# Optimization experiments

Hardware: AMD Instinct MI355X
Metric: run time of the kernel (lower is better)

The kernel has to match this reference:

```python
import jax, jax.numpy as jnp
import numpy as np

B, N, F = 256, 64, 64
S = 2 * N + 2  # seq_len = N*2 + 2 = 130
EPS = 1e-6
SCALE = float(np.sqrt(S))


def _norm(x, alpha, beta):
    # custom Norm: mean/std over last axis, affine params shaped (F, S)
    m = jnp.mean(x, axis=-1, keepdims=True)
    s = jnp.std(x, axis=-1, keepdims=True)
    return alpha * (x - m) / (s + EPS) + beta


def setup_inputs() -> dict:
    key = jax.random.key(0)
    ks = jax.random.split(key, 12)
    d = {
        "sp": jax.random.normal(ks[0], (B, F), jnp.float32),
        "h1": jax.random.normal(ks[1], (B, N, F), jnp.float32),
        "h2": jax.random.normal(ks[2], (B, N, F), jnp.float32),
        # Dense(seq_len) kernels act on last axis of length S
        "Wq": jax.random.normal(ks[3], (S, S), jnp.float32) * 0.05,
        "bq": jnp.zeros((S,), jnp.float32),
        "Wk": jax.random.normal(ks[4], (S, S), jnp.float32) * 0.05,
        "bk": jnp.zeros((S,), jnp.float32),
        "Wv": jax.random.normal(ks[5], (S, S), jnp.float32) * 0.05,
        "bv": jnp.zeros((S,), jnp.float32),
        "alpha1": jnp.ones((F, S), jnp.float32),
        "beta1": jnp.zeros((F, S), jnp.float32),
        "alpha2": jnp.ones((F, S), jnp.float32),
        "beta2": jnp.zeros((F, S), jnp.float32),
        "Wlin": jax.random.normal(ks[6], (F * S, 1), jnp.float32) * 0.02,
        "blin": jnp.zeros((1,), jnp.float32),
    }
    return d


def reference(sp, h1, h2, Wq, bq, Wk, bk, Wv, bv,
              alpha1, beta1, alpha2, beta2, Wlin, blin):
    # obs: (B, 2N+1, F) -> transpose -> (B, F, 2N+1)
    obs = jnp.concatenate((h1, h2, sp[:, None, :]), axis=1).transpose(0, 2, 1)
    h2t = h2.transpose(0, 2, 1)  # (B, F, N): each action is a (B, F) column

    def fwd_action(action):  # action: (B, F)
        x = jnp.concatenate((obs, action[:, :, None]), axis=-1)  # (B, F, S)
        xn = _norm(x, alpha1, beta1)
        q = xn @ Wq + bq  # (B, F, S)
        k = xn @ Wk + bk
        v = xn @ Wv + bv
        # attention over the FEATURE axis: scores (B, F, F)
        sim = jnp.einsum('bis,bjs->bij', q, k) / SCALE
        p = jax.nn.softmax(sim, axis=-1)
        ao = jnp.einsum('bij,bjs->bis', p, v)  # (B, F, S)
        # deterministic dropout => residual is ao + ao
        y = _norm(ao + ao, alpha2, beta2)
        return y.reshape(B, -1) @ Wlin + blin  # (B, 1)

    q_values = jax.vmap(fwd_action, in_axes=-1, out_axes=1)(h2t)  # (B, N, 1)
    return q_values.reshape(B, N)
```

## Files before the change

kernel.cpp:

```cpp
#include <hip/hip_runtime.h>
#include <math.h>


typedef __attribute__((ext_vector_type(4))) float f32x4;
typedef __attribute__((ext_vector_type(8))) _Float16 h8;

#define EPSF 1e-6f
#define INVS 0.0877058019307029f

__device__ __forceinline__ unsigned short f2h(float f) {
  _Float16 h = (_Float16)f;
  return __builtin_bit_cast(unsigned short, h);
}
__device__ __forceinline__ float h2f(unsigned short s) {
  return (float)__builtin_bit_cast(_Float16, s);
}
__device__ __forceinline__ unsigned int pkh(float a, float b) {
  unsigned int r;
  asm("v_cvt_pkrtz_f16_f32 %0, %1, %2" : "=v"(r) : "v"(a), "v"(b));
  return r;
}

__global__ __launch_bounds__(256) void k0(
    const float* __restrict__ alpha1, const float* __restrict__ beta1,
    const float* __restrict__ alpha2, const float* __restrict__ beta2,
    const float* __restrict__ Wq, const float* __restrict__ bq,
    const float* __restrict__ Wk, const float* __restrict__ bk,
    const float* __restrict__ Wv, const float* __restrict__ bv,
    const float* __restrict__ Wlin, const float* __restrict__ blin,
    unsigned short* __restrict__ ABqk, unsigned short* __restrict__ ABv,
    unsigned short* __restrict__ AWt, float* __restrict__ Paw, float* __restrict__ Ccw)
{
  __shared__ float sbuf[64 * 132];
  __shared__ float Wbuf[130 * 144];
  int blk = blockIdx.x, tid = threadIdx.x;
  if (blk < 6) {
    int m = blk >> 1, isB = blk & 1;
    const float* src  = isB ? beta1 : alpha1;
    const float* W    = (m == 0) ? Wq : (m == 1) ? Wk : Wv;
    const float* bias = (m == 0) ? bq : (m == 1) ? bk : bv;
    for (int e = tid; e < 8320; e += 256) { int f = e / 130, s = e - f * 130; sbuf[f * 132 + s] = src[e]; }
    for (int e = tid; e < 16900; e += 256) { int s = e / 130, t = e - s * 130; Wbuf[s * 144 + t] = W[e]; }
    __syncthreads();
    int ty = tid >> 4, tx = tid & 15;
    float acc[4][9] = {};
    for (int s = 0; s < 130; ++s) {
      float g0 = sbuf[(ty * 4 + 0) * 132 + s];
      float g1 = sbuf[(ty * 4 + 1) * 132 + s];
      float g2 = sbuf[(ty * 4 + 2) * 132 + s];
      float g3 = sbuf[(ty * 4 + 3) * 132 + s];
#pragma unroll
      for (int c = 0; c < 9; ++c) {
        float wv = Wbuf[s * 144 + tx + 16 * c];
        acc[0][c] += g0 * wv; acc[1][c] += g1 * wv;
        acc[2][c] += g2 * wv; acc[3][c] += g3 * wv;
      }
    }
#pragma unroll
    for (int i = 0; i < 4; ++i)
      for (int c = 0; c < 9; ++c) {
        int t = tx + 16 * c;
        if (t < 136) {
          float val = (t < 130) ? (acc[i][c] + (isB ? bias[t] : 0.f)) : 0.f;
          unsigned short v16 = f2h(val);
          int f = ty * 4 + i;
          if (m == 2) ABv[t * 128 + isB * 64 + f] = v16;
          else        ABqk[(m * 64 + f) * 272 + (t >> 3) * 16 + isB * 8 + (t & 7)] = v16;
        }
      }
  } else if (blk == 6) {
    if (tid < 64) {
      int f = tid;
      float pa = 0.f, cc = 0.f;
      for (int s = 0; s < 130; ++s) {
        float wl = Wlin[f * 130 + s];
        float aw = alpha2[f * 130 + s] * wl;
        AWt[s * 72 + f] = f2h(aw);
        pa += aw;
        cc += beta2[f * 130 + s] * wl;
      }
      for (int s = 130; s < 144; ++s) AWt[s * 72 + f] = 0;
      Paw[f] = pa;
#pragma unroll
      for (int msk = 1; msk <= 32; msk <<= 1) cc += __shfl_xor(cc, msk, 64);
      if (f == 0) Ccw[0] = cc + blin[0];
    }
  }
}

__global__ __launch_bounds__(256) void k1(
    const float* __restrict__ h1, const float* __restrict__ h2,
    const float* __restrict__ sp, const float* __restrict__ alpha1,
    const float* __restrict__ Wq, const float* __restrict__ Wk, const float* __restrict__ Wv,
    unsigned short* __restrict__ UqkB, unsigned short* __restrict__ UvB,
    float* __restrict__ S1g, float* __restrict__ S2g)
{
  __shared__ float gbuf[64 * 132];
  __shared__ float Wbuf[130 * 144];
  __shared__ float ps[2][256];
  int b = blockIdx.x, tid = threadIdx.x;
  float s1 = 0.f, s2 = 0.f;
  for (int idx = tid; idx < 8256; idx += 256) {
    int s = idx >> 6, f = idx & 63;
    float x = (s < 64)  ? h1[((size_t)(b * 64 + s)) * 64 + f]
            : (s < 128) ? h2[((size_t)(b * 64 + (s - 64))) * 64 + f]
                        : sp[b * 64 + f];
    gbuf[f * 132 + s] = alpha1[f * 130 + s] * x;
    s1 += x; s2 += x * x;
  }
  ps[0][tid] = s1; ps[1][tid] = s2;
  __syncthreads();
  if (tid < 64) {
    S1g[b * 64 + tid] = ps[0][tid] + ps[0][tid + 64] + ps[0][tid + 128] + ps[0][tid + 192];
    S2g[b * 64 + tid] = ps[1][tid] + ps[1][tid + 64] + ps[1][tid + 128] + ps[1][tid + 192];
  }
  int ty = tid >> 4, tx = tid & 15;
  for (int m = 0; m < 3; ++m) {
    const float* W = (m == 0) ? Wq : (m == 1) ? Wk : Wv;
    __syncthreads();
    for (int e = tid; e < 16900; e += 256) { int s = e / 130, t = e - s * 130; Wbuf[s * 144 + t] = W[e]; }
    __syncthreads();
    float acc[4][9] = {};
    for (int s = 0; s < 129; ++s) {
      float g0 = gbuf[(ty * 4 + 0) * 132 + s];
      float g1 = gbuf[(ty * 4 + 1) * 132 + s];
      float g2 = gbuf[(ty * 4 + 2) * 132 + s];
      float g3 = gbuf[(ty * 4 + 3) * 132 + s];
#pragma unroll
      for (int c = 0; c < 9; ++c) {
        float wv = Wbuf[s * 144 + tx + 16 * c];
        acc[0][c] += g0 * wv; acc[1][c] += g1 * wv;
        acc[2][c] += g2 * wv; acc[3][c] += g3 * wv;
      }
    }
#pragma unroll
    for (int i = 0; i < 4; ++i)
      for (int c = 0; c < 9; ++c) {
        int t = tx + 16 * c;
        if (t < 136) {
          unsigned short v16 = f2h((t < 130) ? acc[i][c] : 0.f);
          int f = ty * 4 + i;
          if (m == 2) UvB[((size_t)b * 136 + t) * 64 + f] = v16;
          else        UqkB[(((size_t)b * 2 + m) * 64 + f) * 136 + t] = v16;
        }
      }
  }
}

__global__ __launch_bounds__(512, 2) void k2(
    const float* __restrict__ h2, const float* __restrict__ alpha1,
    const unsigned short* __restrict__ UqkB, const unsigned short* __restrict__ UvB,
    const unsigned short* __restrict__ ABqk, const unsigned short* __restrict__ ABv,
    const unsigned short* __restrict__ AWt,
    const float* __restrict__ S1g, const float* __restrict__ S2g,
    const float* __restrict__ Paw, const float* __restrict__ Ccw,
    const float* __restrict__ Wq, const float* __restrict__ Wk, const float* __restrict__ Wv,
    float* __restrict__ out)
{
  __shared__ __align__(16) unsigned short qb[64 * 168];
  __shared__ __align__(16) unsigned short kb[64 * 168];
  __shared__ __align__(16) unsigned short vT[144 * 72];
  __shared__ __align__(16) unsigned short pb[64 * 72];
  __shared__ __align__(16) unsigned short uqk_l[2 * 64 * 136];
  __shared__ __align__(16) unsigned short uv_l[136 * 64];
  __shared__ __align__(16) unsigned short w129h[3][136];
  __shared__ float S1l[64], S2l[64], ael[64];
  __shared__ __align__(16) unsigned short mrow[64], irow[64], crow[64];
  __shared__ float redbuf[4];

  int b = blockIdx.x, tid = threadIdx.x;
  int w = tid >> 6, l = tid & 63, l15 = l & 15, l4 = l >> 4;

  if (tid < 136) {
    w129h[0][tid] = (tid < 130) ? f2h(Wq[129 * 130 + tid]) : (unsigned short)0;
    w129h[1][tid] = (tid < 130) ? f2h(Wk[129 * 130 + tid]) : (unsigned short)0;
    w129h[2][tid] = (tid < 130) ? f2h(Wv[129 * 130 + tid]) : (unsigned short)0;
  }
  if (tid >= 256 && tid < 320) {
    int ff = tid - 256;
    float s1v = S1g[b * 64 + ff];
    float s2v = S2g[b * 64 + ff];
    float aev = alpha1[ff * 130 + 129];
    S1l[ff] = s1v; S2l[ff] = s2v; ael[ff] = aev;
    float a  = h2[((size_t)(b * 64 + 0)) * 64 + ff];
    float m  = (s1v + a) * (1.f / 130.f);
    float e2 = (s2v + a * a) * (1.f / 130.f);
    float sd = sqrtf(fmaxf(e2 - m * m, 0.f));
    mrow[ff] = f2h(m);
    irow[ff] = f2h(1.f / (sd + EPSF));
    crow[ff] = f2h(aev * a);
  }
  {
    const uint4* src = (const uint4*)(UqkB + ((size_t)b * 2) * 64 * 136);
    uint4* dst = (uint4*)uqk_l;
    for (int i = tid; i < 2176; i += 512) dst[i] = src[i];
  }
  {
    const uint4* src = (const uint4*)(UvB + (size_t)b * 136 * 64);
    uint4* dst = (uint4*)uv_l;
    for (int i = tid; i < 1088; i += 512) dst[i] = src[i];
  }
  for (int i = tid; i < 64 * 24; i += 512) {
    int ff = i / 24, t = 136 + (i - ff * 24);
    qb[ff * 168 + t] = 0; kb[ff * 168 + t] = 0;
  }
  for (int i = tid; i < 14 * 72; i += 512) vT[130 * 72 + i] = 0;

  float awr[9][4], pawr[4];
  if (w < 4) {
#pragma unroll
    for (int sf = 0; sf < 9; ++sf)
#pragma unroll
      for (int rr = 0; rr < 4; ++rr)
        awr[sf][rr] = h2f(AWt[(sf * 16 + l15) * 72 + w * 16 + l4 * 4 + rr]);
#pragma unroll
    for (int rr = 0; rr < 4; ++rr) pawr[rr] = Paw[w * 16 + l4 * 4 + rr];
  }
  float ccv = Ccw[0];

  int isK = tid >> 8, t5 = tid & 255;
  const unsigned short* abg = ABqk + isK * 64 * 272;
  unsigned short* dstqk = isK ? kb : qb;

  __syncthreads();

  auto genqk = [&](int o) {
    int fo = o / 17, g = o - fo * 17;
    _Float16 m = __builtin_bit_cast(_Float16, mrow[fo]);
    _Float16 inv = __builtin_bit_cast(_Float16, irow[fo]);
    _Float16 c = __builtin_bit_cast(_Float16, crow[fo]);
    h8 uu = *(const h8*)(uqk_l + (isK * 64 + fo) * 136 + g * 8);
    h8 aa = *(const h8*)(abg + fo * 272 + g * 16);
    h8 bb = *(const h8*)(abg + fo * 272 + g * 16 + 8);
    h8 ww = *(const h8*)(&w129h[isK][g * 8]);
    h8 res = (uu + c * ww - m * aa) * inv + bb;
    *(h8*)(dstqk + fo * 168 + g * 8) = res;
  };
  auto genv = [&](int o) {
    int t = o >> 3, vf = o & 7;
    _Float16 wv = __builtin_bit_cast(_Float16, w129h[2][t]);
    h8 uu = *(const h8*)(uv_l + t * 64 + vf * 8);
    h8 aa = *(const h8*)(ABv + t * 128 + vf * 8);
    h8 bb = *(const h8*)(ABv + t * 128 + 64 + vf * 8);
    h8 mv = *(const h8*)(&mrow[vf * 8]);
    h8 iv = *(const h8*)(&irow[vf * 8]);
    h8 cv = *(const h8*)(&crow[vf * 8]);
    h8 res = (uu + cv * wv - mv * aa) * iv + bb;
    *(h8*)(&vT[t * 72 + vf * 8]) = res;
  };

  for (int n = 0; n < 64; ++n) {
    if (n > 0 && tid == 0)
      out[b * 64 + n - 1] = redbuf[0] + redbuf[1] + redbuf[2] + redbuf[3] + ccv;
#pragma unroll
    for (int kg = 0; kg < 4; ++kg) genqk(t5 + (kg << 8));
    if (t5 < 64) genqk(1024 + t5);
    genv(tid); genv(tid + 512);
    if (tid < 16) genv(1024 + tid);
    __syncthreads();

    if (w < 4) {
      f32x4 sacc[4] = {};
      {
        const unsigned short* qrow = &qb[(w * 16 + l15) * 168 + l4 * 8];
#pragma unroll
        for (int kk = 0; kk < 5; ++kk) {
          h8 avv = *(const h8*)&qrow[kk * 32];
#pragma unroll
          for (int cf = 0; cf < 4; ++cf) {
            h8 bvv = *(const h8*)&kb[(cf * 16 + l15) * 168 + l4 * 8 + kk * 32];
            sacc[cf] = __builtin_amdgcn_mfma_f32_16x16x32_f16(avv, bvv, sacc[cf], 0, 0, 0);
          }
        }
      }
      float prob[4][4];
#pragma unroll
      for (int rr = 0; rr < 4; ++rr) {
        float ssum = 0.f;
#pragma unroll
        for (int cf = 0; cf < 4; ++cf) {
          float e = __expf(sacc[cf][rr] * INVS);
          prob[cf][rr] = e;
          ssum += e;
        }
#pragma unroll
        for (int msk = 1; msk <= 8; msk <<= 1) ssum += __shfl_xor(ssum, msk, 64);
        float is = 1.f / ssum;
#pragma unroll
        for (int cf = 0; cf < 4; ++cf) prob[cf][rr] *= is;
      }
#pragma unroll
      for (int cf = 0; cf < 4; ++cf) {
        unsigned int p01 = pkh(prob[cf][0], prob[cf][1]);
        unsigned int p23 = pkh(prob[cf][2], prob[cf][3]);
        int base = (w * 16 + l4 * 4) * 72 + cf * 16 + l15;
        pb[base]       = (unsigned short)p01;
        pb[base + 72]  = (unsigned short)(p01 >> 16);
        pb[base + 144] = (unsigned short)p23;
        pb[base + 216] = (unsigned short)(p23 >> 16);
      }

      f32x4 ao[9] = {};
      {
        const unsigned short* prow = &pb[(w * 16 + l15) * 72 + l4 * 8];
#pragma unroll
        for (int kk = 0; kk < 2; ++kk) {
          h8 avv = *(const h8*)&prow[kk * 32];
#pragma unroll
          for (int sf = 0; sf < 9; ++sf) {
            h8 bvv = *(const h8*)&vT[(sf * 16 + l15) * 72 + l4 * 8 + kk * 32];
            ao[sf] = __builtin_amdgcn_mfma_f32_16x16x32_f16(avv, bvv, ao[sf], 0, 0, 0);
          }
        }
      }
      float csum = 0.f;
#pragma unroll
      for (int rr = 0; rr < 4; ++rr) {
        float s1 = 0.f, s2 = 0.f, sdt = 0.f;
#pragma unroll
        for (int sf = 0; sf < 9; ++sf) {
          float v = ao[sf][rr];
          s1 += v; s2 += v * v; sdt += v * awr[sf][rr];
        }
#pragma unroll
        for (int msk = 1; msk <= 8; msk <<= 1) {
          s1 += __shfl_xor(s1, msk, 64);
          s2 += __shfl_xor(s2, msk, 64);
          sdt += __shfl_xor(sdt, msk, 64);
        }
        float mz  = 2.f * s1 * (1.f / 130.f);
        float ez2 = 4.f * s2 * (1.f / 130.f);
        float sg  = sqrtf(fmaxf(ez2 - mz * mz, 0.f));
        float i2  = 1.f / (sg + EPSF);
        csum += (2.f * sdt - mz * pawr[rr]) * i2;
      }
      csum += __shfl_xor(csum, 16, 64);
      csum += __shfl_xor(csum, 32, 64);
      if (l == 0) redbuf[w] = csum;
    } else if (w == 4 && n < 63) {
      int ff = l;
      float a  = h2[((size_t)(b * 64 + n + 1)) * 64 + ff];
      float m  = (S1l[ff] + a) * (1.f / 130.f);
      float e2 = (S2l[ff] + a * a) * (1.f / 130.f);
      float sd = sqrtf(fmaxf(e2 - m * m, 0.f));
      mrow[ff] = f2h(m);
      irow[ff] = f2h(1.f / (sd + EPSF));
      crow[ff] = f2h(ael[ff] * a);
    }
    __syncthreads();
  }
  if (tid == 0)
    out[b * 64 + 63] = redbuf[0] + redbuf[1] + redbuf[2] + redbuf[3] + ccv;
}

extern "C" void kernel_launch(void* const* d_in, const int* in_sizes, int n_in,
                              void* d_out, int out_size, void* d_ws, size_t ws_size,
                              hipStream_t stream) {
  const float* sp     = (const float*)d_in[0];
  const float* h1     = (const float*)d_in[1];
  const float* h2     = (const float*)d_in[2];
  const float* Wq     = (const float*)d_in[3];
  const float* bq     = (const float*)d_in[4];
  const float* Wk     = (const float*)d_in[5];
  const float* bk     = (const float*)d_in[6];
  const float* Wv     = (const float*)d_in[7];
  const float* bv     = (const float*)d_in[8];
  const float* alpha1 = (const float*)d_in[9];
  const float* beta1  = (const float*)d_in[10];
  const float* alpha2 = (const float*)d_in[11];
  const float* beta2  = (const float*)d_in[12];
  const float* Wlin   = (const float*)d_in[13];
  const float* blin   = (const float*)d_in[14];
  float* out = (float*)d_out;

  unsigned short* UqkB = (unsigned short*)d_ws;
  unsigned short* UvB  = UqkB + 4456448;
  unsigned short* ABqk = UvB + 2228224;
  unsigned short* ABv  = ABqk + 34816;
  unsigned short* AWt  = ABv + 17408;
  float* S1g = (float*)(AWt + 10368);
  float* S2g = S1g + 16384;
  float* Paw = S2g + 16384;
  float* Ccw = Paw + 64;

  k0<<<dim3(7), dim3(256), 0, stream>>>(alpha1, beta1, alpha2, beta2,
                                        Wq, bq, Wk, bk, Wv, bv, Wlin, blin,
                                        ABqk, ABv, AWt, Paw, Ccw);
  k1<<<dim3(256), dim3(256), 0, stream>>>(h1, h2, sp, alpha1, Wq, Wk, Wv,
                                          UqkB, UvB, S1g, S2g);
  k2<<<dim3(256), dim3(512), 0, stream>>>(h2, alpha1, UqkB, UvB, ABqk, ABv, AWt,
                                          S1g, S2g, Paw, Ccw,
                                          Wq, Wk, Wv, out);
}
```

Baseline: 327.3 us.

## Split k2 action loop across two blocks per batch and keep U/AB operands in registers

The main kernel now launches two blocks per batch row, each handling 32 of the 64 actions, so 512 blocks instead of 256 fill the GPU's compute units better. The per-batch U and AB operands used to build q/k/v are loaded once into registers before the loop instead of being staged in shared memory and reread every iteration. This cuts LDS footprint and per-iteration LDS reads. The cost is duplicated setup loads per block and higher register pressure under the 512-thread, 2-blocks-per-CU launch bound, which could cause spills.

Measured after the change: 343.5 us. +5.0%, slower.

```diff
diff --git a/kernel.cpp b/kernel.cpp
--- a/kernel.cpp
+++ b/kernel.cpp
@@ -161,14 +161,14 @@
   __shared__ __align__(16) unsigned short kb[64 * 168];
   __shared__ __align__(16) unsigned short vT[144 * 72];
   __shared__ __align__(16) unsigned short pb[64 * 72];
-  __shared__ __align__(16) unsigned short uqk_l[2 * 64 * 136];
-  __shared__ __align__(16) unsigned short uv_l[136 * 64];
   __shared__ __align__(16) unsigned short w129h[3][136];
   __shared__ float S1l[64], S2l[64], ael[64];
   __shared__ __align__(16) unsigned short mrow[64], irow[64], crow[64];
   __shared__ float redbuf[4];
 
-  int b = blockIdx.x, tid = threadIdx.x;
+  int bh = blockIdx.x;
+  int b = bh >> 1, n0 = (bh & 1) << 5;
+  int tid = threadIdx.x;
   int w = tid >> 6, l = tid & 63, l15 = l & 15, l4 = l >> 4;
 
   if (tid < 136) {
@@ -182,23 +182,13 @@
     float s2v = S2g[b * 64 + ff];
     float aev = alpha1[ff * 130 + 129];
     S1l[ff] = s1v; S2l[ff] = s2v; ael[ff] = aev;
-    float a  = h2[((size_t)(b * 64 + 0)) * 64 + ff];
+    float a  = h2[((size_t)(b * 64 + n0)) * 64 + ff];
     float m  = (s1v + a) * (1.f / 130.f);
     float e2 = (s2v + a * a) * (1.f / 130.f);
     float sd = sqrtf(fmaxf(e2 - m * m, 0.f));
     mrow[ff] = f2h(m);
     irow[ff] = f2h(1.f / (sd + EPSF));
-    crow[ff] = f2h(aev * a);
-  }
-  {
-    const uint4* src = (const uint4*)(UqkB + ((size_t)b * 2) * 64 * 136);
-    uint4* dst = (uint4*)uqk_l;
-    for (int i = tid; i < 2176; i += 512) dst[i] = src[i];
-  }
-  {
-    const uint4* src = (const uint4*)(UvB + (size_t)b * 136 * 64);
-    uint4* dst = (uint4*)uv_l;
-    for (int i = tid; i < 1088; i += 512) dst[i] = src[i];
+    crow[ff] = f2h(ael[ff] * a);
   }
   for (int i = tid; i < 64 * 24; i += 512) {
     int ff = i / 24, t = 136 + (i - ff * 24);
@@ -219,29 +209,48 @@
   float ccv = Ccw[0];
 
   int isK = tid >> 8, t5 = tid & 255;
-  const unsigned short* abg = ABqk + isK * 64 * 272;
+  const unsigned short* uqkg = UqkB + ((size_t)b * 2 + isK) * 64 * 136;
+  const unsigned short* abg  = ABqk + isK * 64 * 272;
+  const unsigned short* uvg  = UvB + (size_t)b * 136 * 64;
   unsigned short* dstqk = isK ? kb : qb;
 
+  auto ldu = [&](int o) { int fo = o / 17, g = o - fo * 17;
+                          return *(const h8*)(uqkg + fo * 136 + g * 8); };
+  auto lda = [&](int o) { int fo = o / 17, g = o - fo * 17;
+                          return *(const h8*)(abg + fo * 272 + g * 16); };
+  auto ldb = [&](int o) { int fo = o / 17, g = o - fo * 17;
+                          return *(const h8*)(abg + fo * 272 + g * 16 + 8); };
+  h8 qU0 = ldu(t5),       qA0 = lda(t5),       qB0 = ldb(t5);
+  h8 qU1 = ldu(t5 + 256), qA1 = lda(t5 + 256), qB1 = ldb(t5 + 256);
+  h8 qU2 = ldu(t5 + 512), qA2 = lda(t5 + 512), qB2 = ldb(t5 + 512);
+  h8 qU3 = ldu(t5 + 768), qA3 = lda(t5 + 768), qB3 = ldb(t5 + 768);
+  h8 qUt = {}, qAt = {}, qBt = {};
+  if (t5 < 64) { qUt = ldu(1024 + t5); qAt = lda(1024 + t5); qBt = ldb(1024 + t5); }
+  auto ldvu = [&](int o) { int t = o >> 3, vf = o & 7;
+                           return *(const h8*)(uvg + t * 64 + vf * 8); };
+  auto ldva = [&](int o) { int t = o >> 3, vf = o & 7;
+                           return *(const h8*)(ABv + t * 128 + (o & 7) * 8); };
+  auto ldvb = [&](int o) { int t = o >> 3;
+                           return *(const h8*)(ABv + t * 128 + 64 + (o & 7) * 8); };
+  h8 vU0 = ldvu(tid),       vA0 = ldva(tid),       vB0 = ldvb(tid);
+  h8 vU1 = ldvu(tid + 512), vA1 = ldva(tid + 512), vB1 = ldvb(tid + 512);
+  h8 vUt = {}, vAt = {}, vBt = {};
+  if (tid < 16) { vUt = ldvu(1024 + tid); vAt = ldva(1024 + tid); vBt = ldvb(1024 + tid); }
+
   __syncthreads();
 
-  auto genqk = [&](int o) {
+  auto genqk = [&](int o, h8 uu, h8 aa, h8 bb) {
     int fo = o / 17, g = o - fo * 17;
-    _Float16 m = __builtin_bit_cast(_Float16, mrow[fo]);
+    _Float16 m   = __builtin_bit_cast(_Float16, mrow[fo]);
     _Float16 inv = __builtin_bit_cast(_Float16, irow[fo]);
-    _Float16 c = __builtin_bit_cast(_Float16, crow[fo]);
-    h8 uu = *(const h8*)(uqk_l + (isK * 64 + fo) * 136 + g * 8);
-    h8 aa = *(const h8*)(abg + fo * 272 + g * 16);
-    h8 bb = *(const h8*)(abg + fo * 272 + g * 16 + 8);
+    _Float16 c   = __builtin_bit_cast(_Float16, crow[fo]);
     h8 ww = *(const h8*)(&w129h[isK][g * 8]);
     h8 res = (uu + c * ww - m * aa) * inv + bb;
     *(h8*)(dstqk + fo * 168 + g * 8) = res;
   };
-  auto genv = [&](int o) {
+  auto genv = [&](int o, h8 uu, h8 aa, h8 bb) {
     int t = o >> 3, vf = o & 7;
     _Float16 wv = __builtin_bit_cast(_Float16, w129h[2][t]);
-    h8 uu = *(const h8*)(uv_l + t * 64 + vf * 8);
-    h8 aa = *(const h8*)(ABv + t * 128 + vf * 8);
-    h8 bb = *(const h8*)(ABv + t * 128 + 64 + vf * 8);
     h8 mv = *(const h8*)(&mrow[vf * 8]);
     h8 iv = *(const h8*)(&irow[vf * 8]);
     h8 cv = *(const h8*)(&crow[vf * 8]);
@@ -249,14 +258,17 @@
     *(h8*)(&vT[t * 72 + vf * 8]) = res;
   };
 
-  for (int n = 0; n < 64; ++n) {
-    if (n > 0 && tid == 0)
+  for (int n = n0; n < n0 + 32; ++n) {
+    if (n > n0 && tid == 0)
       out[b * 64 + n - 1] = redbuf[0] + redbuf[1] + redbuf[2] + redbuf[3] + ccv;
-#pragma unroll
-    for (int kg = 0; kg < 4; ++kg) genqk(t5 + (kg << 8));
-    if (t5 < 64) genqk(1024 + t5);
-    genv(tid); genv(tid + 512);
-    if (tid < 16) genv(1024 + tid);
+    genqk(t5,       qU0, qA0, qB0);
+    genqk(t5 + 256, qU1, qA1, qB1);
+    genqk(t5 + 512, qU2, qA2, qB2);
+    genqk(t5 + 768, qU3, qA3, qB3);
+    if (t5 < 64) genqk(1024 + t5, qUt, qAt, qBt);
+    genv(tid,       vU0, vA0, vB0);
+    genv(tid + 512, vU1, vA1, vB1);
+    if (tid < 16) genv(1024 + tid, vUt, vAt, vBt);
     __syncthreads();
 
     if (w < 4) {
@@ -337,7 +349,7 @@
       csum += __shfl_xor(csum, 16, 64);
       csum += __shfl_xor(csum, 32, 64);
       if (l == 0) redbuf[w] = csum;
-    } else if (w == 4 && n < 63) {
+    } else if (w == 4 && n < n0 + 31) {
       int ff = l;
       float a  = h2[((size_t)(b * 64 + n + 1)) * 64 + ff];
       float m  = (S1l[ff] + a) * (1.f / 130.f);
@@ -350,7 +362,7 @@
     __syncthreads();
   }
   if (tid == 0)
-    out[b * 64 + 63] = redbuf[0] + redbuf[1] + redbuf[2] + redbuf[3] + ccv;
+    out[b * 64 + n0 + 31] = redbuf[0] + redbuf[1] + redbuf[2] + redbuf[3] + ccv;
 }
 
 extern "C" void kernel_launch(void* const* d_in, const int* in_sizes, int n_in,
@@ -388,7 +400,7 @@
                                         ABqk, ABv, AWt, Paw, Ccw);
   k1<<<dim3(256), dim3(256), 0, stream>>>(h1, h2, sp, alpha1, Wq, Wk, Wv,
                                           UqkB, UvB, S1g, S2g);
-  k2<<<dim3(256), dim3(512), 0, stream>>>(h2, alpha1, UqkB, UvB, ABqk, ABv, AWt,
+  k2<<<dim3(512), dim3(512), 0, stream>>>(h2, alpha1, UqkB, UvB, ABqk, ABv, AWt,
                                           S1g, S2g, Paw, Ccw,
                                           Wq, Wk, Wv, out);
 }
```

## Split k2 across four blocks per batch and keep U operands in registers

Applied to the files above, without the earlier changes.

k2 now launches 1024 blocks of 256 threads, and each block handles 16 of the 64 actions for one batch element instead of all 64. The per-action norm statistics are computed up front for all 16 actions, which removes the dedicated warp that prepared the next action. The U slices for q, k and v are loaded straight from global memory into registers rather than staged in LDS, which cuts shared-memory use and allows more blocks per CU. In exchange each block reloads the U data and weights, so global traffic for them rises fourfold and register pressure grows.

New measurement: 383.6 us. +17.2%, slower.

```diff
diff --git a/kernel.cpp b/kernel.cpp
--- a/kernel.cpp
+++ b/kernel.cpp
@@ -147,7 +147,7 @@
   }
 }
 
-__global__ __launch_bounds__(512, 2) void k2(
+__global__ __launch_bounds__(256, 2) void k2(
     const float* __restrict__ h2, const float* __restrict__ alpha1,
     const unsigned short* __restrict__ UqkB, const unsigned short* __restrict__ UvB,
     const unsigned short* __restrict__ ABqk, const unsigned short* __restrict__ ABv,
@@ -161,14 +161,15 @@
   __shared__ __align__(16) unsigned short kb[64 * 168];
   __shared__ __align__(16) unsigned short vT[144 * 72];
   __shared__ __align__(16) unsigned short pb[64 * 72];
-  __shared__ __align__(16) unsigned short uqk_l[2 * 64 * 136];
-  __shared__ __align__(16) unsigned short uv_l[136 * 64];
   __shared__ __align__(16) unsigned short w129h[3][136];
-  __shared__ float S1l[64], S2l[64], ael[64];
-  __shared__ __align__(16) unsigned short mrow[64], irow[64], crow[64];
+  __shared__ __align__(16) unsigned short mrowA[16][64];
+  __shared__ __align__(16) unsigned short irowA[16][64];
+  __shared__ __align__(16) unsigned short crowA[16][64];
   __shared__ float redbuf[4];
 
-  int b = blockIdx.x, tid = threadIdx.x;
+  int bh = blockIdx.x;
+  int b = bh >> 2, n0 = (bh & 3) << 4;
+  int tid = threadIdx.x;
   int w = tid >> 6, l = tid & 63, l15 = l & 15, l4 = l >> 4;
 
   if (tid < 136) {
@@ -176,90 +177,112 @@
     w129h[1][tid] = (tid < 130) ? f2h(Wk[129 * 130 + tid]) : (unsigned short)0;
     w129h[2][tid] = (tid < 130) ? f2h(Wv[129 * 130 + tid]) : (unsigned short)0;
   }
-  if (tid >= 256 && tid < 320) {
-    int ff = tid - 256;
+  for (int idx = tid; idx < 16 * 64; idx += 256) {
+    int nn = idx >> 6, ff = idx & 63;
+    float a   = h2[((size_t)(b * 64 + n0 + nn)) * 64 + ff];
     float s1v = S1g[b * 64 + ff];
     float s2v = S2g[b * 64 + ff];
     float aev = alpha1[ff * 130 + 129];
-    S1l[ff] = s1v; S2l[ff] = s2v; ael[ff] = aev;
-    float a  = h2[((size_t)(b * 64 + 0)) * 64 + ff];
-    float m  = (s1v + a) * (1.f / 130.f);
-    float e2 = (s2v + a * a) * (1.f / 130.f);
-    float sd = sqrtf(fmaxf(e2 - m * m, 0.f));
-    mrow[ff] = f2h(m);
-    irow[ff] = f2h(1.f / (sd + EPSF));
-    crow[ff] = f2h(aev * a);
-  }
-  {
-    const uint4* src = (const uint4*)(UqkB + ((size_t)b * 2) * 64 * 136);
-    uint4* dst = (uint4*)uqk_l;
-    for (int i = tid; i < 2176; i += 512) dst[i] = src[i];
-  }
-  {
-    const uint4* src = (const uint4*)(UvB + (size_t)b * 136 * 64);
-    uint4* dst = (uint4*)uv_l;
-    for (int i = tid; i < 1088; i += 512) dst[i] = src[i];
-  }
-  for (int i = tid; i < 64 * 24; i += 512) {
+    float m   = (s1v + a) * (1.f / 130.f);
+    float e2  = (s2v + a * a) * (1.f / 130.f);
+    float sd  = sqrtf(fmaxf(e2 - m * m, 0.f));
+    mrowA[nn][ff] = f2h(m);
+    irowA[nn][ff] = f2h(1.f / (sd + EPSF));
+    crowA[nn][ff] = f2h(aev * a);
+  }
+  for (int i = tid; i < 64 * 24; i += 256) {
     int ff = i / 24, t = 136 + (i - ff * 24);
     qb[ff * 168 + t] = 0; kb[ff * 168 + t] = 0;
   }
-  for (int i = tid; i < 14 * 72; i += 512) vT[130 * 72 + i] = 0;
+  for (int i = tid; i < 14 * 72; i += 256) vT[130 * 72 + i] = 0;
 
   float awr[9][4], pawr[4];
-  if (w < 4) {
-#pragma unroll
-    for (int sf = 0; sf < 9; ++sf)
-#pragma unroll
-      for (int rr = 0; rr < 4; ++rr)
-        awr[sf][rr] = h2f(AWt[(sf * 16 + l15) * 72 + w * 16 + l4 * 4 + rr]);
-#pragma unroll
-    for (int rr = 0; rr < 4; ++rr) pawr[rr] = Paw[w * 16 + l4 * 4 + rr];
-  }
+#pragma unroll
+  for (int sf = 0; sf < 9; ++sf)
+#pragma unroll
+    for (int rr = 0; rr < 4; ++rr)
+      awr[sf][rr] = h2f(AWt[(sf * 16 + l15) * 72 + w * 16 + l4 * 4 + rr]);
+#pragma unroll
+  for (int rr = 0; rr < 4; ++rr) pawr[rr] = Paw[w * 16 + l4 * 4 + rr];
   float ccv = Ccw[0];
 
-  int isK = tid >> 8, t5 = tid & 255;
-  const unsigned short* abg = ABqk + isK * 64 * 272;
-  unsigned short* dstqk = isK ? kb : qb;
+  const unsigned short* uqg = UqkB + ((size_t)b * 2 + 0) * 64 * 136;
+  const unsigned short* ukg = UqkB + ((size_t)b * 2 + 1) * 64 * 136;
+  const unsigned short* uvg = UvB + (size_t)b * 136 * 64;
+  auto ldu = [&](const unsigned short* base, int o) {
+    int fo = o / 17, g = o - fo * 17;
+    return *(const h8*)(base + fo * 136 + g * 8);
+  };
+  auto ldvu = [&](int o) {
+    int t = o >> 3, vf = o & 7;
+    return *(const h8*)(uvg + t * 64 + vf * 8);
+  };
+  h8 qU0 = ldu(uqg, tid),       qU1 = ldu(uqg, tid + 256);
+  h8 qU2 = ldu(uqg, tid + 512), qU3 = ldu(uqg, tid + 768);
+  h8 kU0 = ldu(ukg, tid),       kU1 = ldu(ukg, tid + 256);
+  h8 kU2 = ldu(ukg, tid + 512), kU3 = ldu(ukg, tid + 768);
+  h8 qUt = {}, kUt = {};
+  if (tid < 64) { qUt = ldu(uqg, 1024 + tid); kUt = ldu(ukg, 1024 + tid); }
+  h8 vU0 = ldvu(tid),       vU1 = ldvu(tid + 256);
+  h8 vU2 = ldvu(tid + 512), vU3 = ldvu(tid + 768);
+  h8 vUt = {};
+  if (tid < 16) vUt = ldvu(1024 + tid);
 
   __syncthreads();
 
-  auto genqk = [&](int o) {
-    int fo = o / 17, g = o - fo * 17;
-    _Float16 m = __builtin_bit_cast(_Float16, mrow[fo]);
-    _Float16 inv = __builtin_bit_cast(_Float16, irow[fo]);
-    _Float16 c = __builtin_bit_cast(_Float16, crow[fo]);
-    h8 uu = *(const h8*)(uqk_l + (isK * 64 + fo) * 136 + g * 8);
-    h8 aa = *(const h8*)(abg + fo * 272 + g * 16);
-    h8 bb = *(const h8*)(abg + fo * 272 + g * 16 + 8);
-    h8 ww = *(const h8*)(&w129h[isK][g * 8]);
-    h8 res = (uu + c * ww - m * aa) * inv + bb;
-    *(h8*)(dstqk + fo * 168 + g * 8) = res;
-  };
-  auto genv = [&](int o) {
-    int t = o >> 3, vf = o & 7;
-    _Float16 wv = __builtin_bit_cast(_Float16, w129h[2][t]);
-    h8 uu = *(const h8*)(uv_l + t * 64 + vf * 8);
-    h8 aa = *(const h8*)(ABv + t * 128 + vf * 8);
-    h8 bb = *(const h8*)(ABv + t * 128 + 64 + vf * 8);
-    h8 mv = *(const h8*)(&mrow[vf * 8]);
-    h8 iv = *(const h8*)(&irow[vf * 8]);
-    h8 cv = *(const h8*)(&crow[vf * 8]);
-    h8 res = (uu + cv * wv - mv * aa) * iv + bb;
-    *(h8*)(&vT[t * 72 + vf * 8]) = res;
-  };
-
-  for (int n = 0; n < 64; ++n) {
-    if (n > 0 && tid == 0)
-      out[b * 64 + n - 1] = redbuf[0] + redbuf[1] + redbuf[2] + redbuf[3] + ccv;
-#pragma unroll
-    for (int kg = 0; kg < 4; ++kg) genqk(t5 + (kg << 8));
-    if (t5 < 64) genqk(1024 + t5);
-    genv(tid); genv(tid + 512);
-    if (tid < 16) genv(1024 + tid);
+  for (int ni = 0; ni < 16; ++ni) {
+    if (ni > 0 && tid == 0)
+      out[b * 64 + n0 + ni - 1] = redbuf[0] + redbuf[1] + redbuf[2] + redbuf[3] + ccv;
+    {
+      const unsigned short* mr = mrowA[ni];
+      const unsigned short* ir = irowA[ni];
+      const unsigned short* cr = crowA[ni];
+      auto genqk = [&](int o, h8 uu, const unsigned short* abg_, int wrow,
+                       unsigned short* dstb) {
+        int fo = o / 17, g = o - fo * 17;
+        _Float16 m   = __builtin_bit_cast(_Float16, mr[fo]);
+        _Float16 inv = __builtin_bit_cast(_Float16, ir[fo]);
+        _Float16 c   = __builtin_bit_cast(_Float16, cr[fo]);
+        h8 aa = *(const h8*)(abg_ + fo * 272 + g * 16);
+        h8 bb = *(const h8*)(abg_ + fo * 272 + g * 16 + 8);
+        h8 ww = *(const h8*)(&w129h[wrow][g * 8]);
+        h8 res = (uu + c * ww - m * aa) * inv + bb;
+        *(h8*)(dstb + fo * 168 + g * 8) = res;
+      };
+      auto genv = [&](int o, h8 uu) {
+        int t = o >> 3, vf = o & 7;
+        _Float16 wv = __builtin_bit_cast(_Float16, w129h[2][t]);
+        h8 aa = *(const h8*)(ABv + t * 128 + vf * 8);
+        h8 bb = *(const h8*)(ABv + t * 128 + 64 + vf * 8);
+        h8 mv = *(const h8*)(&mr[vf * 8]);
+        h8 iv = *(const h8*)(&ir[vf * 8]);
+        h8 cv = *(const h8*)(&cr[vf * 8]);
+        h8 res = (uu + cv * wv - mv * aa) * iv + bb;
+        *(h8*)(&vT[t * 72 + vf * 8]) = res;
+      };
+      const unsigned short* abq = ABqk;
+      const unsigned short* abk = ABqk + 64 * 272;
+      genqk(tid,       qU0, abq, 0, qb);
+      genqk(tid + 256, qU1, abq, 0, qb);
+      genqk(tid + 512, qU2, abq, 0, qb);
+      genqk(tid + 768, qU3, abq, 0, qb);
+      genqk(tid,       kU0, abk, 1, kb);
+      genqk(tid + 256, kU1, abk, 1, kb);
+      genqk(tid + 512, kU2, abk, 1, kb);
+      genqk(tid + 768, kU3, abk, 1, kb);
+      if (tid < 64) {
+        genqk(1024 + tid, qUt, abq, 0, qb);
+        genqk(1024 + tid, kUt, abk, 1, kb);
+      }
+      genv(tid,       vU0);
+      genv(tid + 256, vU1);
+      genv(tid + 512, vU2);
+      genv(tid + 768, vU3);
+      if (tid < 16) genv(1024 + tid, vUt);
+    }
     __syncthreads();
 
-    if (w < 4) {
+    {
       f32x4 sacc[4] = {};
       {
         const unsigned short* qrow = &qb[(w * 16 + l15) * 168 + l4 * 8];
@@ -337,20 +360,11 @@
       csum += __shfl_xor(csum, 16, 64);
       csum += __shfl_xor(csum, 32, 64);
       if (l == 0) redbuf[w] = csum;
-    } else if (w == 4 && n < 63) {
-      int ff = l;
-      float a  = h2[((size_t)(b * 64 + n + 1)) * 64 + ff];
-      float m  = (S1l[ff] + a) * (1.f / 130.f);
-      float e2 = (S2l[ff] + a * a) * (1.f / 130.f);
-      float sd = sqrtf(fmaxf(e2 - m * m, 0.f));
-      mrow[ff] = f2h(m);
-      irow[ff] = f2h(1.f / (sd + EPSF));
-      crow[ff] = f2h(ael[ff] * a);
     }
     __syncthreads();
   }
   if (tid == 0)
-    out[b * 64 + 63] = redbuf[0] + redbuf[1] + redbuf[2] + redbuf[3] + ccv;
+    out[b * 64 + n0 + 15] = redbuf[0] + redbuf[1] + redbuf[2] + redbuf[3] + ccv;
 }
 
 extern "C" void kernel_launch(void* const* d_in, const int* in_sizes, int n_in,
@@ -388,7 +402,7 @@
                                         ABqk, ABv, AWt, Paw, Ccw);
   k1<<<dim3(256), dim3(256), 0, stream>>>(h1, h2, sp, alpha1, Wq, Wk, Wv,
                                           UqkB, UvB, S1g, S2g);
-  k2<<<dim3(256), dim3(512), 0, stream>>>(h2, alpha1, UqkB, UvB, ABqk, ABv, AWt,
-                                          S1g, S2g, Paw, Ccw,
-                                          Wq, Wk, Wv, out);
-}
+  k2<<<dim3(1024), dim3(256), 0, stream>>>(h2, alpha1, UqkB, UvB, ABqk, ABv, AWt,
+                                           S1g, S2g, Paw, Ccw,
+                                           Wq, Wk, Wv, out);
+}
```
